# Optimization experiments

Hardware: AMD Instinct MI355X
Metric: run time of the kernel (lower is better)

The kernel has to match this reference:

```python
import jax, jax.numpy as jnp
import numpy as np

B, M, K = 8, 4096, 16
C = 64       # input_dim
D = 64       # d_model


def _lin(key, fan_in, fan_out):
    k1, k2 = jax.random.split(key)
    bound = 1.0 / np.sqrt(fan_in)
    W = jax.random.uniform(k1, (fan_out, fan_in), minval=-bound, maxval=bound, dtype=jnp.float32)
    b = jax.random.uniform(k2, (fan_out,), minval=-bound, maxval=bound, dtype=jnp.float32)
    return W, b


def setup_inputs() -> dict:
    key = jax.random.key(0)
    ks = jax.random.split(key, 12)
    x = jax.random.normal(ks[0], (B, M, K, C), dtype=jnp.float32)
    xyz = jax.random.normal(ks[1], (B, M, K, 3), dtype=jnp.float32)
    Wq, bq = _lin(ks[2], C, D)
    Wk, bk = _lin(ks[3], C, D)
    Wv, bv = _lin(ks[4], C, D)
    Wp1, bp1 = _lin(ks[5], 3, D)
    Wp2, bp2 = _lin(ks[6], D, D)
    Wa1, ba1 = _lin(ks[7], D, D)
    Wa2, ba2 = _lin(ks[8], D, D)
    W2, b2 = _lin(ks[9], D, C)
    return dict(x=x, xyz=xyz, Wq=Wq, bq=bq, Wk=Wk, bk=bk, Wv=Wv, bv=bv,
                Wp1=Wp1, bp1=bp1, Wp2=Wp2, bp2=bp2,
                Wa1=Wa1, ba1=ba1, Wa2=Wa2, ba2=ba2, W2=W2, b2=b2)


def reference(x, xyz, Wq, bq, Wk, bk, Wv, bv, Wp1, bp1, Wp2, bp2,
              Wa1, ba1, Wa2, ba2, W2, b2):
    lin = lambda t, W, b: jnp.matmul(t, W.T) + b
    raw_feature = x[:, :, 0, :]                 # [B,M,C]
    raw_xyz = xyz[:, :, 0:1, :]                 # [B,M,1,3]
    q = lin(raw_feature, Wq, bq)                # [B,M,D]
    k = lin(x, Wk, bk)                          # [B,M,K,D]
    v = lin(x, Wv, bv)                          # [B,M,K,D]
    rel = xyz - raw_xyz                         # [B,M,K,3]
    pos_enc = lin(jax.nn.relu(lin(rel, Wp1, bp1)), Wp2, bp2)  # [B,M,K,D]
    h = q[:, :, None, :] - k + pos_enc          # [B,M,K,D]
    attn_logits = lin(jax.nn.relu(lin(h, Wa1, ba1)), Wa2, ba2)
    attn = jax.nn.softmax(attn_logits / np.sqrt(D), axis=-2)  # softmax over K
    res = jnp.einsum('bmnf,bmnf->bmf', attn, v + pos_enc)
    return lin(res, W2, b2) + raw_feature       # [B,M,C]
```

## Files before the change

kernel.cpp:

```cpp
#include <hip/hip_runtime.h>

#define NM 4096
#define NK 16
#define NC 64

typedef __attribute__((ext_vector_type(8))) short s8v;
typedef __attribute__((ext_vector_type(4))) float f4v;
typedef __attribute__((ext_vector_type(2))) unsigned int u2v;

__device__ __forceinline__ short f2bf(float f) {
  unsigned u = __builtin_bit_cast(unsigned, f);
  u += 0x7fffu + ((u >> 16) & 1u);
  return (short)(u >> 16);
}
__device__ __forceinline__ float bf2f(unsigned short s) {
  return __builtin_bit_cast(float, ((unsigned)s) << 16);
}
__device__ __forceinline__ unsigned pk2(float a, float b) {
  return (unsigned)(unsigned short)f2bf(a) | ((unsigned)(unsigned short)f2bf(b) << 16);
}
__device__ __forceinline__ s8v pack8(f4v a, f4v b) {
  s8v r;
  r[0]=f2bf(a[0]); r[1]=f2bf(a[1]); r[2]=f2bf(a[2]); r[3]=f2bf(a[3]);
  r[4]=f2bf(b[0]); r[5]=f2bf(b[1]); r[6]=f2bf(b[2]); r[7]=f2bf(b[3]);
  return r;
}

#define MFMA(a,b,c) __builtin_amdgcn_mfma_f32_16x16x32_bf16((a),(b),(c),0,0,0)

#define HSTRIDE 72
#define TB (16*HSTRIDE)

__global__ void precomp_kernel(const float* __restrict__ Wq, const float* __restrict__ bq,
                               const float* __restrict__ Wk, const float* __restrict__ bk,
                               const float* __restrict__ Wp2,const float* __restrict__ bp2,
                               const float* __restrict__ Wa1,const float* __restrict__ ba1,
                               float* __restrict__ ws) {
  const int gid = blockIdx.x * 256 + threadIdx.x;
  if (gid < 3*4096) {
    const int m = gid >> 12, e = gid & 4095, i = e >> 6, j = e & 63;
    const float* R = Wa1 + i*64;
    float s = 0.f;
    if (m == 0)      { for (int l = 0; l < 64; ++l) s += R[l] * Wq [l*64 + j]; }
    else if (m == 1) { for (int l = 0; l < 64; ++l) s -= R[l] * Wk [l*64 + j]; }
    else             { for (int l = 0; l < 64; ++l) s += R[l] * Wp2[l*64 + j]; }
    ws[gid] = s;
  } else if (gid < 3*4096 + 64) {
    const int i = gid - 3*4096;
    const float* R = Wa1 + i*64;
    float s = 0.f;
    for (int l = 0; l < 64; ++l) s += R[l] * bq[l];
    ws[gid] = s;
  } else if (gid < 3*4096 + 128) {
    const int i = gid - (3*4096 + 64);
    const float* R = Wa1 + i*64;
    float s = ba1[i];
    for (int l = 0; l < 64; ++l) s += R[l] * (bp2[l] - bk[l]);
    ws[gid] = s;
  }
}

__global__ __attribute__((amdgpu_flat_work_group_size(256, 256)))
           __attribute__((amdgpu_waves_per_eu(1, 8)))
void lattn_kernel(const float* __restrict__ x,  const float* __restrict__ xyz,
                  const float* __restrict__ Wp1,const float* __restrict__ bp1,
                  const float* __restrict__ Wp2,const float* __restrict__ bp2,
                  const float* __restrict__ Wv, const float* __restrict__ bv,
                  const float* __restrict__ Wa2,const float* __restrict__ ba2,
                  const float* __restrict__ W2, const float* __restrict__ b2,
                  const float* __restrict__ ws,
                  float* __restrict__ out) {
  __shared__ __align__(16) short wlds[5*8*64*8];
  __shared__ __align__(16) short qres[4*TB];
  __shared__ __align__(16) short hbuf[4*TB];

  const int tid = threadIdx.x;
  const float* wak = ws + 4096;
  const float* wap = ws + 8192;
  const float* bqa = ws + 12288;
  const float* bcv = ws + 12352;

  for (int idx = tid; idx < 5*8*64; idx += 256) {
    const int mat = idx >> 9;
    const int rem = idx & 511;
    const int f   = rem >> 6;
    const int ln  = rem & 63;
    const int t = f >> 1, h = f & 1;
    const int cc = ln & 15, qq = ln >> 4;
    const int n = 16*t + cc;
    const float* W = (mat==0) ? wak : (mat==1) ? Wv : (mat==2) ? Wp2 : (mat==3) ? wap : Wa2;
    const bool prm = (mat >= 2);
    s8v v;
    #pragma unroll
    for (int j = 0; j < 8; ++j) {
      int kp = h*32 + qq*8 + j;
      int k = prm ? (((kp & 3) << 4) | (kp >> 2)) : kp;
      v[j] = f2bf(W[n*64 + k]);
    }
    *(s8v*)&wlds[(size_t)idx * 8] = v;
  }
  __syncthreads();

  const int w    = tid >> 6;
  const int lane = tid & 63;
  const int c    = lane & 15;
  const int lq   = lane >> 4;

  const int gw  = blockIdx.x * 4 + w;
  const int gp0 = gw << 4;
  const int b   = gp0 >> 12;
  const int m0  = gp0 & (NM - 1);

  short* qbuf = qres + w * TB;
  short* hb   = hbuf + w * TB;

  float wp1c[4][3];
  float bp1f[4], bvf[4], bp2f[4], ba2f[4], bcf[4];
  #pragma unroll
  for (int t = 0; t < 4; ++t) {
    const int n = 16*t + c;
    wp1c[t][0] = Wp1[n*3+0]; wp1c[t][1] = Wp1[n*3+1]; wp1c[t][2] = Wp1[n*3+2];
    bp1f[t] = bp1[n]; bvf[t] = bv[n]; bp2f[t] = bp2[n];
    ba2f[t] = ba2[n]; bcf[t] = bcv[n];
  }

  const long ptbase = (long)(b * NM + m0);

  {
    const float* xr = x + (ptbase + c) * (long)(NK*NC) + 8*lq;
    s8v rA0 = pack8(*(const f4v*)xr,        *(const f4v*)(xr+4));
    s8v rA1 = pack8(*(const f4v*)(xr+32),   *(const f4v*)(xr+36));
    #pragma unroll
    for (int t = 0; t < 4; ++t) {
      const float* wr = ws + (16*t + c)*64 + 8*lq;
      s8v w0 = pack8(*(const f4v*)wr,       *(const f4v*)(wr+4));
      s8v w1 = pack8(*(const f4v*)(wr+32),  *(const f4v*)(wr+36));
      const float bb = bqa[16*t + c];
      f4v acc = {bb, bb, bb, bb};
      acc = MFMA(rA0, w0, acc);
      acc = MFMA(rA1, w1, acc);
      #pragma unroll
      for (int r = 0; r < 4; ++r)
        qbuf[(4*lq + r)*HSTRIDE + 16*t + c] = f2bf(acc[r]);
    }
  }

  f4v nxr0, nxr1, nxr2, nxr3;
  float nza[3], nzb[3];
  {
    const float* xr = x + ptbase * (long)(NK*NC) + c*NC + 8*lq;
    nxr0 = *(const f4v*)xr;      nxr1 = *(const f4v*)(xr+4);
    nxr2 = *(const f4v*)(xr+32); nxr3 = *(const f4v*)(xr+36);
    const float* zp = xyz + ptbase * (long)(NK*3);
    nza[0] = zp[c*3+0]; nza[1] = zp[c*3+1]; nza[2] = zp[c*3+2];
    nzb[0] = zp[0];     nzb[1] = zp[1];     nzb[2] = zp[2];
  }

  #pragma unroll 1
  for (int p = 0; p < 16; ++p) {
    s8v xA0 = pack8(nxr0, nxr1);
    s8v xA1 = pack8(nxr2, nxr3);
    const float rx = nza[0] - nzb[0];
    const float ry = nza[1] - nzb[1];
    const float rz = nza[2] - nzb[2];
    if (p < 15) {
      const long prow = ptbase + p + 1;
      const float* xr = x + prow * (long)(NK*NC) + c*NC + 8*lq;
      nxr0 = *(const f4v*)xr;      nxr1 = *(const f4v*)(xr+4);
      nxr2 = *(const f4v*)(xr+32); nxr3 = *(const f4v*)(xr+36);
      const float* zp = xyz + prow * (long)(NK*3);
      nza[0] = zp[c*3+0]; nza[1] = zp[c*3+1]; nza[2] = zp[c*3+2];
      nzb[0] = zp[0];     nzb[1] = zp[1];     nzb[2] = zp[2];
    }

    f4v s[4];
    #pragma unroll
    for (int t = 0; t < 4; ++t) {
      const short* wb = &wlds[(0*512 + 2*t*64 + lane) * 8];
      s8v w0 = *(const s8v*)wb;
      s8v w1 = *(const s8v*)(wb + 512);
      const float base = bf2f((unsigned short)qbuf[p*HSTRIDE + 16*t + c]) + bcf[t];
      f4v acc = {base, base, base, base};
      acc = MFMA(xA0, w0, acc);
      acc = MFMA(xA1, w1, acc);
      s[t] = acc;
    }

    {
      float rxs[4], rys[4], rzs[4];
      #pragma unroll
      for (int r = 0; r < 4; ++r) {
        rxs[r] = __shfl(rx, 4*lq + r);
        rys[r] = __shfl(ry, 4*lq + r);
        rzs[r] = __shfl(rz, 4*lq + r);
      }
      f4v p1[4];
      #pragma unroll
      for (int t = 0; t < 4; ++t)
        #pragma unroll
        for (int r = 0; r < 4; ++r) {
          float v = bp1f[t] + wp1c[t][0]*rxs[r] + wp1c[t][1]*rys[r] + wp1c[t][2]*rzs[r];
          p1[t][r] = fmaxf(v, 0.0f);
        }
      #pragma unroll
      for (int r = 0; r < 4; ++r) {
        u2v pv = { pk2(p1[0][r], p1[1][r]), pk2(p1[2][r], p1[3][r]) };
        *(u2v*)&hb[(4*lq + r)*HSTRIDE + 4*c] = pv;
      }
    }
    s8v pA0 = *(const s8v*)&hb[c*HSTRIDE + 8*lq];
    s8v pA1 = *(const s8v*)&hb[c*HSTRIDE + 32 + 8*lq];

    f4v pe[4];
    #pragma unroll
    for (int t = 0; t < 4; ++t) {
      const short* wb = &wlds[(2*512 + 2*t*64 + lane) * 8];
      s8v w0 = *(const s8v*)wb;
      s8v w1 = *(const s8v*)(wb + 512);
      f4v acc = {bp2f[t], bp2f[t], bp2f[t], bp2f[t]};
      acc = MFMA(pA0, w0, acc);
      acc = MFMA(pA1, w1, acc);
      pe[t] = acc;
    }

    #pragma unroll
    for (int t = 0; t < 4; ++t) {
      const short* wb = &wlds[(3*512 + 2*t*64 + lane) * 8];
      s8v w0 = *(const s8v*)wb;
      s8v w1 = *(const s8v*)(wb + 512);
      f4v acc = MFMA(pA0, w0, s[t]);
      acc = MFMA(pA1, w1, acc);
      #pragma unroll
      for (int r = 0; r < 4; ++r) s[t][r] = fmaxf(acc[r], 0.0f);
    }
    #pragma unroll
    for (int r = 0; r < 4; ++r) {
      u2v pv = { pk2(s[0][r], s[1][r]), pk2(s[2][r], s[3][r]) };
      *(u2v*)&hb[(4*lq + r)*HSTRIDE + 4*c] = pv;
    }
    s8v aA0 = *(const s8v*)&hb[c*HSTRIDE + 8*lq];
    s8v aA1 = *(const s8v*)&hb[c*HSTRIDE + 32 + 8*lq];

    f4v vacc[4];
    #pragma unroll
    for (int t = 0; t < 4; ++t) {
      const short* wb = &wlds[(1*512 + 2*t*64 + lane) * 8];
      s8v w0 = *(const s8v*)wb;
      s8v w1 = *(const s8v*)(wb + 512);
      f4v acc = {bvf[t], bvf[t], bvf[t], bvf[t]};
      acc = MFMA(xA0, w0, acc);
      acc = MFMA(xA1, w1, acc);
      vacc[t] = acc;
    }

    f4v lg[4];
    #pragma unroll
    for (int t = 0; t < 4; ++t) {
      const short* wb = &wlds[(4*512 + 2*t*64 + lane) * 8];
      s8v w0 = *(const s8v*)wb;
      s8v w1 = *(const s8v*)(wb + 512);
      f4v acc = {ba2f[t], ba2f[t], ba2f[t], ba2f[t]};
      acc = MFMA(aA0, w0, acc);
      acc = MFMA(aA1, w1, acc);
      lg[t] = acc;
    }

    #pragma unroll
    for (int t = 0; t < 4; ++t) {
      f4v l = lg[t];
      float mx = fmaxf(fmaxf(l[0], l[1]), fmaxf(l[2], l[3]));
      mx = fmaxf(mx, __shfl_xor(mx, 16));
      mx = fmaxf(mx, __shfl_xor(mx, 32));
      f4v e;
      #pragma unroll
      for (int r = 0; r < 4; ++r) e[r] = exp2f((l[r] - mx) * 0.18033688011112043f);
      float sm = e[0] + e[1] + e[2] + e[3];
      sm += __shfl_xor(sm, 16);
      sm += __shfl_xor(sm, 32);
      const float ri = 1.0f / sm;
      float pr = 0.0f;
      #pragma unroll
      for (int r = 0; r < 4; ++r) pr += (e[r] * ri) * (vacc[t][r] + pe[t][r]);
      pr += __shfl_xor(pr, 16);
      pr += __shfl_xor(pr, 32);
      if (lq == 0) qbuf[p*HSTRIDE + 16*t + c] = f2bf(pr);
    }
  }

  {
    s8v resA0 = *(const s8v*)&qbuf[c*HSTRIDE + 8*lq];
    s8v resA1 = *(const s8v*)&qbuf[c*HSTRIDE + 32 + 8*lq];
    #pragma unroll
    for (int t = 0; t < 4; ++t) {
      const float* wr = W2 + (16*t + c)*64 + 8*lq;
      s8v w0 = pack8(*(const f4v*)wr,      *(const f4v*)(wr+4));
      s8v w1 = pack8(*(const f4v*)(wr+32), *(const f4v*)(wr+36));
      const float bb = b2[16*t + c];
      f4v acc = {bb, bb, bb, bb};
      acc = MFMA(resA0, w0, acc);
      acc = MFMA(resA1, w1, acc);
      #pragma unroll
      for (int r = 0; r < 4; ++r) {
        const long pr2 = ptbase + 4*lq + r;
        out[pr2*NC + 16*t + c] = acc[r] + x[pr2*(long)(NK*NC) + 16*t + c];
      }
    }
  }
}

extern "C" void kernel_launch(void* const* d_in, const int* in_sizes, int n_in,
                              void* d_out, int out_size, void* d_ws, size_t ws_size,
                              hipStream_t stream) {
  (void)in_sizes; (void)n_in; (void)out_size; (void)ws_size;
  const float* x   = (const float*)d_in[0];
  const float* xyz = (const float*)d_in[1];
  const float* Wq  = (const float*)d_in[2];
  const float* bq  = (const float*)d_in[3];
  const float* Wk  = (const float*)d_in[4];
  const float* bk  = (const float*)d_in[5];
  const float* Wv  = (const float*)d_in[6];
  const float* bv  = (const float*)d_in[7];
  const float* Wp1 = (const float*)d_in[8];
  const float* bp1 = (const float*)d_in[9];
  const float* Wp2 = (const float*)d_in[10];
  const float* bp2 = (const float*)d_in[11];
  const float* Wa1 = (const float*)d_in[12];
  const float* ba1 = (const float*)d_in[13];
  const float* Wa2 = (const float*)d_in[14];
  const float* ba2 = (const float*)d_in[15];
  const float* W2  = (const float*)d_in[16];
  const float* b2  = (const float*)d_in[17];
  float* out = (float*)d_out;
  float* ws  = (float*)d_ws;

  precomp_kernel<<<dim3(49), dim3(256), 0, stream>>>(Wq, bq, Wk, bk, Wp2, bp2, Wa1, ba1, ws);
  lattn_kernel<<<dim3(512), dim3(256), 0, stream>>>(
      x, xyz, Wp1, bp1, Wp2, bp2, Wv, bv, Wa2, ba2, W2, b2, ws, out);
}
```

Measured before the change: 294.9 us.

## Compute pos-enc hidden directly in MFMA operand layout and fuse v with pos_enc

Each lane now computes the relu(Wp1·rel+bp1) values directly in the A-operand layout the MFMA needs, using per-lane preloaded weight vectors. This removes the shuffles, the LDS write/read round trip and the extra pos-enc MFMA pass. The v and pos_enc projections are merged into one accumulator chain with a combined bias, softmax normalisation is deferred until after the reduction, and bf16 conversion uses the compiler intrinsic. In exchange, the 16 preloaded f4v weight registers raise register pressure, and pos_enc is no longer kept separately.

```diff
diff --git a/kernel.cpp b/kernel.cpp
--- a/kernel.cpp
+++ b/kernel.cpp
@@ -9,15 +9,15 @@
 typedef __attribute__((ext_vector_type(2))) unsigned int u2v;
 
 __device__ __forceinline__ short f2bf(float f) {
-  unsigned u = __builtin_bit_cast(unsigned, f);
-  u += 0x7fffu + ((u >> 16) & 1u);
-  return (short)(u >> 16);
+  return __builtin_bit_cast(short, (__bf16)f);
 }
 __device__ __forceinline__ float bf2f(unsigned short s) {
   return __builtin_bit_cast(float, ((unsigned)s) << 16);
 }
 __device__ __forceinline__ unsigned pk2(float a, float b) {
-  return (unsigned)(unsigned short)f2bf(a) | ((unsigned)(unsigned short)f2bf(b) << 16);
+  unsigned short lo = __builtin_bit_cast(unsigned short, (__bf16)a);
+  unsigned short hi = __builtin_bit_cast(unsigned short, (__bf16)b);
+  return (unsigned)lo | ((unsigned)hi << 16);
 }
 __device__ __forceinline__ s8v pack8(f4v a, f4v b) {
   s8v r;
@@ -114,13 +114,20 @@
   short* qbuf = qres + w * TB;
   short* hb   = hbuf + w * TB;
 
-  float wp1c[4][3];
-  float bp1f[4], bvf[4], bp2f[4], ba2f[4], bcf[4];
+  f4v wp1v[16];
+  #pragma unroll
+  for (int i = 0; i < 16; ++i) {
+    const int jj = i & 7, h = i >> 3;
+    const int n = 16*(jj&3) + 2*lq + (jj>>2) + 8*h;
+    f4v t4;
+    t4[0] = Wp1[n*3+0]; t4[1] = Wp1[n*3+1]; t4[2] = Wp1[n*3+2]; t4[3] = bp1[n];
+    wp1v[i] = t4;
+  }
+  float bvpe[4], ba2f[4], bcf[4];
   #pragma unroll
   for (int t = 0; t < 4; ++t) {
     const int n = 16*t + c;
-    wp1c[t][0] = Wp1[n*3+0]; wp1c[t][1] = Wp1[n*3+1]; wp1c[t][2] = Wp1[n*3+2];
-    bp1f[t] = bp1[n]; bvf[t] = bv[n]; bp2f[t] = bp2[n];
+    bvpe[t] = bv[n] + bp2[n];
     ba2f[t] = ba2[n]; bcf[t] = bcv[n];
   }
 
@@ -186,41 +193,14 @@
       s[t] = acc;
     }
 
-    {
-      float rxs[4], rys[4], rzs[4];
-      #pragma unroll
-      for (int r = 0; r < 4; ++r) {
-        rxs[r] = __shfl(rx, 4*lq + r);
-        rys[r] = __shfl(ry, 4*lq + r);
-        rzs[r] = __shfl(rz, 4*lq + r);
-      }
-      f4v p1[4];
-      #pragma unroll
-      for (int t = 0; t < 4; ++t)
-        #pragma unroll
-        for (int r = 0; r < 4; ++r) {
-          float v = bp1f[t] + wp1c[t][0]*rxs[r] + wp1c[t][1]*rys[r] + wp1c[t][2]*rzs[r];
-          p1[t][r] = fmaxf(v, 0.0f);
-        }
-      #pragma unroll
-      for (int r = 0; r < 4; ++r) {
-        u2v pv = { pk2(p1[0][r], p1[1][r]), pk2(p1[2][r], p1[3][r]) };
-        *(u2v*)&hb[(4*lq + r)*HSTRIDE + 4*c] = pv;
-      }
-    }
-    s8v pA0 = *(const s8v*)&hb[c*HSTRIDE + 8*lq];
-    s8v pA1 = *(const s8v*)&hb[c*HSTRIDE + 32 + 8*lq];
-
-    f4v pe[4];
-    #pragma unroll
-    for (int t = 0; t < 4; ++t) {
-      const short* wb = &wlds[(2*512 + 2*t*64 + lane) * 8];
-      s8v w0 = *(const s8v*)wb;
-      s8v w1 = *(const s8v*)(wb + 512);
-      f4v acc = {bp2f[t], bp2f[t], bp2f[t], bp2f[t]};
-      acc = MFMA(pA0, w0, acc);
-      acc = MFMA(pA1, w1, acc);
-      pe[t] = acc;
+    s8v pA0, pA1;
+    #pragma unroll
+    for (int i = 0; i < 8; ++i) {
+      f4v w0v = wp1v[i], w1v = wp1v[8+i];
+      float v0 = fmaxf(fmaf(w0v[0], rx, fmaf(w0v[1], ry, fmaf(w0v[2], rz, w0v[3]))), 0.0f);
+      float v1 = fmaxf(fmaf(w1v[0], rx, fmaf(w1v[1], ry, fmaf(w1v[2], rz, w1v[3]))), 0.0f);
+      pA0[i] = f2bf(v0);
+      pA1[i] = f2bf(v1);
     }
 
     #pragma unroll
@@ -238,20 +218,22 @@
       u2v pv = { pk2(s[0][r], s[1][r]), pk2(s[2][r], s[3][r]) };
       *(u2v*)&hb[(4*lq + r)*HSTRIDE + 4*c] = pv;
     }
+
+    f4v vpe[4];
+    #pragma unroll
+    for (int t = 0; t < 4; ++t) {
+      const short* wb1 = &wlds[(1*512 + 2*t*64 + lane) * 8];
+      const short* wb2 = &wlds[(2*512 + 2*t*64 + lane) * 8];
+      f4v acc = {bvpe[t], bvpe[t], bvpe[t], bvpe[t]};
+      acc = MFMA(xA0, *(const s8v*)wb1, acc);
+      acc = MFMA(xA1, *(const s8v*)(wb1 + 512), acc);
+      acc = MFMA(pA0, *(const s8v*)wb2, acc);
+      acc = MFMA(pA1, *(const s8v*)(wb2 + 512), acc);
+      vpe[t] = acc;
+    }
+
     s8v aA0 = *(const s8v*)&hb[c*HSTRIDE + 8*lq];
     s8v aA1 = *(const s8v*)&hb[c*HSTRIDE + 32 + 8*lq];
-
-    f4v vacc[4];
-    #pragma unroll
-    for (int t = 0; t < 4; ++t) {
-      const short* wb = &wlds[(1*512 + 2*t*64 + lane) * 8];
-      s8v w0 = *(const s8v*)wb;
-      s8v w1 = *(const s8v*)(wb + 512);
-      f4v acc = {bvf[t], bvf[t], bvf[t], bvf[t]};
-      acc = MFMA(xA0, w0, acc);
-      acc = MFMA(xA1, w1, acc);
-      vacc[t] = acc;
-    }
 
     f4v lg[4];
     #pragma unroll
@@ -277,12 +259,12 @@
       float sm = e[0] + e[1] + e[2] + e[3];
       sm += __shfl_xor(sm, 16);
       sm += __shfl_xor(sm, 32);
-      const float ri = 1.0f / sm;
       float pr = 0.0f;
       #pragma unroll
-      for (int r = 0; r < 4; ++r) pr += (e[r] * ri) * (vacc[t][r] + pe[t][r]);
+      for (int r = 0; r < 4; ++r) pr += e[r] * vpe[t][r];
       pr += __shfl_xor(pr, 16);
       pr += __shfl_xor(pr, 32);
+      pr *= 1.0f / sm;
       if (lq == 0) qbuf[p*HSTRIDE + 16*t + c] = f2bf(pr);
     }
   }
```

Result: faster. 277.7 us (-5.9%).
